# Kernel optimization log

Measured on AMD Instinct MI355X. Metric: run time of the kernel, lower is better.

The kernel has to match this reference:

```python
import jax, jax.numpy as jnp
import numpy as np

EMBED_DIM = 1024
NUM_HEADS = 16
HEAD_DIM = EMBED_DIM // NUM_HEADS


def setup_inputs() -> dict:
    key = jax.random.key(0)
    k1, k2, k3, k4, k5 = jax.random.split(key, 5)
    B, S, D = 1, 4096, EMBED_DIM
    scale = 0.02
    return {
        "input": jax.random.normal(k1, (B, S, D), dtype=jnp.float32),
        "Wqkv": jax.random.normal(k2, (D, 3 * D), dtype=jnp.float32) * scale,
        "bqkv": jax.random.normal(k3, (3 * D,), dtype=jnp.float32) * scale,
        "Wo": jax.random.normal(k4, (D, D), dtype=jnp.float32) * scale,
        "bo": jax.random.normal(k5, (D,), dtype=jnp.float32) * scale,
    }


def reference(input, Wqkv, bqkv, Wo, bo):
    B, S, D = input.shape
    H, Hd = NUM_HEADS, HEAD_DIM
    qkv = input @ Wqkv + bqkv                        # [B, S, 3D]
    qkv = qkv.reshape(B, S, 3, H, Hd)
    qkv = jnp.transpose(qkv, (2, 0, 3, 1, 4))        # [3, B, H, S, Hd]
    q, k, v = qkv[0], qkv[1], qkv[2]
    scores = jnp.einsum("bhsd,bhtd->bhst", q, k) / (Hd ** 0.5)  # [B,H,S,S]
    causal = jnp.tril(jnp.ones((S, S), dtype=bool))[None, None]
    scores = jnp.where(causal, scores, -jnp.inf)
    attn = jax.nn.softmax(scores, axis=-1)
    out = jnp.einsum("bhst,bhtd->bhsd", attn, v)     # [B,H,S,Hd]
    out = jnp.transpose(out, (0, 2, 1, 3)).reshape(B, S, D)
    return out @ Wo + bo
```

## Files before the change

### kernel.cpp

```cpp
#include <hip/hip_runtime.h>

typedef __bf16 bf16;
typedef __bf16 bf16x8 __attribute__((ext_vector_type(8)));
typedef float f32x4 __attribute__((ext_vector_type(4)));
typedef float f32x16 __attribute__((ext_vector_type(16)));
typedef unsigned u32x2 __attribute__((ext_vector_type(2)));

#define MFMA16(a, b, c) __builtin_amdgcn_mfma_f32_16x16x32_bf16((a), (b), (c), 0, 0, 0)
#define MFMA32(a, b, c) __builtin_amdgcn_mfma_f32_32x32x16_bf16((a), (b), (c), 0, 0, 0)

typedef const __attribute__((address_space(1))) uint32_t glb_u32;
typedef __attribute__((address_space(3))) uint32_t lds_u32;
#define GLOAD16(gp, lp) __builtin_amdgcn_global_load_lds((glb_u32*)(gp), (lds_u32*)(lp), 16, 0, 0)

__global__ __launch_bounds__(256) void k_prep(const float* __restrict__ X, bf16* __restrict__ Xb,
                                              const float* __restrict__ Wqkv, bf16* __restrict__ WqkvT,
                                              const float* __restrict__ Wo, bf16* __restrict__ WoT) {
    __shared__ float tile[64][65];
    int bid = blockIdx.x;
    int t = threadIdx.x;
    if (bid < 2048) {
        size_t i = ((size_t)bid * 256 + t) * 8;
        float4 a = *(const float4*)(X + i);
        float4 b = *(const float4*)(X + i + 4);
        bf16 e[8];
        e[0] = (bf16)a.x; e[1] = (bf16)a.y; e[2] = (bf16)a.z; e[3] = (bf16)a.w;
        e[4] = (bf16)b.x; e[5] = (bf16)b.y; e[6] = (bf16)b.z; e[7] = (bf16)b.w;
        uint4 u; __builtin_memcpy(&u, e, 16);
        *(uint4*)(Xb + i) = u;
        return;
    }
    const float* in; bf16* out; int R, C, bx, by;
    if (bid < 2816) {
        in = Wqkv; out = WqkvT; R = 1024; C = 3072;
        int b = bid - 2048; bx = b % 48; by = b / 48;
    } else {
        in = Wo; out = WoT; R = 1024; C = 1024;
        int b = bid - 2816; bx = b & 15; by = b >> 4;
    }
    for (int i = 0; i < 16; ++i) {
        int e = i * 256 + t; int r = e >> 6, c = e & 63;
        tile[r][c] = in[(size_t)(by * 64 + r) * C + bx * 64 + c];
    }
    __syncthreads();
    for (int i = 0; i < 16; ++i) {
        int e = i * 256 + t; int r = e >> 6, c = e & 63;
        out[(size_t)(bx * 64 + r) * R + by * 64 + c] = (bf16)tile[c][r];
    }
}

__device__ __forceinline__ void gemm128_core(const bf16* __restrict__ A, const bf16* __restrict__ Bt,
                                             int r0, int c0, int Kd, char* As, char* Bs,
                                             f32x4 (&acc)[4][4]) {
    int t = threadIdx.x, l = t & 63, w = t >> 6;
    int g = l >> 4, li = l & 15;
    int wr = w >> 1, wc = w & 1;
    for (int k0 = 0; k0 < Kd; k0 += 64) {
        __syncthreads();
        #pragma unroll
        for (int i = 0; i < 4; ++i) {
            int slot = i * 256 + t;
            int row = slot >> 3;
            int ch  = (slot & 7) ^ (row & 7);
            int base = (i * 256 + w * 64) * 16;
            GLOAD16(A  + (size_t)(r0 + row) * Kd + k0 + ch * 8, As + base);
            GLOAD16(Bt + (size_t)(c0 + row) * Kd + k0 + ch * 8, Bs + base);
        }
        __syncthreads();
        __builtin_amdgcn_s_setprio(1);
        #pragma unroll
        for (int kk = 0; kk < 2; ++kk) {
            bf16x8 af[4], bfr[4];
            #pragma unroll
            for (int m = 0; m < 4; ++m) {
                int row = wr * 64 + m * 16 + li;
                af[m] = *(const bf16x8*)(As + ((row * 128 + kk * 64 + g * 16) ^ ((row & 7) << 4)));
            }
            #pragma unroll
            for (int n = 0; n < 4; ++n) {
                int row = wc * 64 + n * 16 + li;
                bfr[n] = *(const bf16x8*)(Bs + ((row * 128 + kk * 64 + g * 16) ^ ((row & 7) << 4)));
            }
            #pragma unroll
            for (int m = 0; m < 4; ++m)
                #pragma unroll
                for (int n = 0; n < 4; ++n)
                    acc[m][n] = MFMA16(af[m], bfr[n], acc[m][n]);
        }
        __builtin_amdgcn_s_setprio(0);
    }
}

__global__ __launch_bounds__(256) void k_gemm_qkv(const bf16* __restrict__ Xb, const bf16* __restrict__ WqkvT,
                                                  const float* __restrict__ bqkv,
                                                  bf16* __restrict__ Q, bf16* __restrict__ Kfr,
                                                  bf16* __restrict__ Vfr) {
    __shared__ __align__(16) char As[16384];
    __shared__ __align__(16) char Bs[16384];
    int bid = blockIdx.x;
    int Lg = (bid & 7) * 96 + (bid >> 3);
    int bx = Lg % 24, by = Lg / 24;
    int r0 = by * 128, c0 = bx * 128;
    f32x4 acc[4][4] = {};
    gemm128_core(Xb, WqkvT, r0, c0, 1024, As, Bs, acc);
    int t = threadIdx.x, l = t & 63, w = t >> 6;
    int g = l >> 4, li = l & 15;
    int wr = w >> 1, wc = w & 1;
    int colbase = c0 + wc * 64;
    int sec = colbase >> 10;
    int head = (colbase & 1023) >> 6;
    if (sec == 0) {
        const float scale = 0.125f * 1.44269504f;
        #pragma unroll
        for (int m = 0; m < 4; ++m)
            #pragma unroll
            for (int n = 0; n < 4; ++n) {
                int hd = n * 16 + li;
                float bias = bqkv[colbase + hd];
                #pragma unroll
                for (int r = 0; r < 4; ++r) {
                    int row = r0 + wr * 64 + m * 16 + g * 4 + r;
                    Q[(size_t)(head * 4096 + row) * 64 + hd] = (bf16)((acc[m][n][r] + bias) * scale);
                }
            }
    } else if (sec == 1) {
        bf16* dstK = Kfr + (size_t)head * 262144;
        #pragma unroll
        for (int m = 0; m < 4; ++m) {
            int tbase = r0 + wr * 64 + m * 16 + g * 4;
            size_t tpart = (size_t)(tbase >> 5) * 2048 + (size_t)(tbase & 31) * 8;
            #pragma unroll
            for (int n = 0; n < 4; ++n) {
                int hd = n * 16 + li;
                float bias = bqkv[colbase + hd];
                size_t A0 = tpart + (size_t)(hd >> 4) * 512 + (size_t)((hd >> 3) & 1) * 256 + (hd & 7);
                #pragma unroll
                for (int r = 0; r < 4; ++r)
                    dstK[A0 + (size_t)r * 8] = (bf16)(acc[m][n][r] + bias);
            }
        }
    } else {
        bf16* dstV = Vfr + (size_t)head * 262144;
        #pragma unroll
        for (int m = 0; m < 4; ++m) {
            int tbase = r0 + wr * 64 + m * 16 + g * 4;
            size_t tpart = (size_t)(tbase >> 5) * 2048 + (size_t)((tbase >> 4) & 1) * 512
                         + (size_t)((tbase >> 3) & 1) * 256 + (tbase & 7);
            #pragma unroll
            for (int n = 0; n < 4; ++n) {
                int hd = n * 16 + li;
                float bias = bqkv[colbase + hd];
                size_t A0 = tpart + (size_t)(hd >> 5) * 1024 + (size_t)(hd & 31) * 8;
                bf16 e4[4];
                #pragma unroll
                for (int r = 0; r < 4; ++r) e4[r] = (bf16)(acc[m][n][r] + bias);
                unsigned long long pk; __builtin_memcpy(&pk, e4, 8);
                *(unsigned long long*)(dstV + A0) = pk;
            }
        }
    }
}

__global__ __launch_bounds__(256) void k_gemm_out(const bf16* __restrict__ Ob, const bf16* __restrict__ WoT,
                                                  const float* __restrict__ bo, float* __restrict__ out) {
    __shared__ __align__(16) char As[16384];
    __shared__ __align__(16) char Bs[8192];
    int bid = blockIdx.x;
    int Lg = (bid & 7) * 64 + (bid >> 3);
    int bx = Lg & 15, by = Lg >> 4;
    int r0 = by * 128, c0 = bx * 64;
    int t = threadIdx.x, l = t & 63, w = t >> 6;
    int g = l >> 4, li = l & 15;
    f32x4 acc[2][4] = {};
    for (int k0 = 0; k0 < 1024; k0 += 64) {
        __syncthreads();
        #pragma unroll
        for (int i = 0; i < 4; ++i) {
            int slot = i * 256 + t;
            int row = slot >> 3;
            int ch  = (slot & 7) ^ (row & 7);
            int base = (i * 256 + w * 64) * 16;
            GLOAD16(Ob + (size_t)(r0 + row) * 1024 + k0 + ch * 8, As + base);
        }
        #pragma unroll
        for (int i = 0; i < 2; ++i) {
            int slot = i * 256 + t;
            int row = slot >> 3;
            int ch  = (slot & 7) ^ (row & 7);
            int base = (i * 256 + w * 64) * 16;
            GLOAD16(WoT + (size_t)(c0 + row) * 1024 + k0 + ch * 8, Bs + base);
        }
        __syncthreads();
        __builtin_amdgcn_s_setprio(1);
        #pragma unroll
        for (int kk = 0; kk < 2; ++kk) {
            bf16x8 af[2], bfr[4];
            #pragma unroll
            for (int m = 0; m < 2; ++m) {
                int row = w * 32 + m * 16 + li;
                af[m] = *(const bf16x8*)(As + ((row * 128 + kk * 64 + g * 16) ^ ((row & 7) << 4)));
            }
            #pragma unroll
            for (int n = 0; n < 4; ++n) {
                int row = n * 16 + li;
                bfr[n] = *(const bf16x8*)(Bs + ((row * 128 + kk * 64 + g * 16) ^ ((row & 7) << 4)));
            }
            #pragma unroll
            for (int m = 0; m < 2; ++m)
                #pragma unroll
                for (int n = 0; n < 4; ++n)
                    acc[m][n] = MFMA16(af[m], bfr[n], acc[m][n]);
        }
        __builtin_amdgcn_s_setprio(0);
    }
    #pragma unroll
    for (int m = 0; m < 2; ++m)
        #pragma unroll
        for (int n = 0; n < 4; ++n) {
            int col = c0 + n * 16 + li;
            float bias = bo[col];
            #pragma unroll
            for (int r = 0; r < 4; ++r) {
                int row = r0 + w * 32 + m * 16 + g * 4 + r;
                out[(size_t)row * 1024 + col] = acc[m][n][r] + bias;
            }
        }
}

__device__ __forceinline__ unsigned pkbf(float a, float b) {
    bf16 h0 = (bf16)a, h1 = (bf16)b;
    unsigned short u0, u1;
    __builtin_memcpy(&u0, &h0, 2); __builtin_memcpy(&u1, &h1, 2);
    return (unsigned)u0 | ((unsigned)u1 << 16);
}

__global__ __launch_bounds__(128) void k_attn(const bf16* __restrict__ Q, const uint4* __restrict__ Kfr,
                                              const uint4* __restrict__ Vfr, bf16* __restrict__ O) {
    __shared__ float Op[32][64];
    __shared__ float Ls[32];
    int bid = blockIdx.x;
    int h = bid & 15;
    int u = bid >> 4;
    int jj = (u < 64) ? u : 191 - u;
    int w = threadIdx.x >> 6;
    int l = threadIdx.x & 63;
    int lc = l & 31, hi = l >> 5;
    int hi4 = hi * 4, hi8 = hi * 8;
    const bf16* Qh = Q + (size_t)h * 4096 * 64;
    const uint4* Kh = Kfr + (size_t)h * 32768;
    const uint4* Vh = Vfr + (size_t)h * 32768;
    int nt = jj + 1;
    int hA = (nt + 1) >> 1;
    int tb = w ? hA : 0;
    int te = w ? nt : hA;

    f32x16 oacc[2] = {};
    float lsum = 0.f;
    uint4 kA[4], vA[4], kB[4], vB[4];
    bf16x8 qf[4];
    #pragma unroll
    for (int kst = 0; kst < 4; ++kst)
        qf[kst] = *(const bf16x8*)(Qh + (size_t)(jj * 32 + lc) * 64 + kst * 16 + hi8);

    auto compute = [&](int tt, uint4 (&kf)[4], uint4 (&vf)[4]) {
        f32x16 sacc = {};
        __builtin_amdgcn_s_setprio(1);
        #pragma unroll
        for (int kst = 0; kst < 4; ++kst) {
            bf16x8 kk; __builtin_memcpy(&kk, &kf[kst], 16);
            sacc = MFMA32(kk, qf[kst], sacc);
        }
        __builtin_amdgcn_s_setprio(0);
        if (tt == jj) {
            #pragma unroll
            for (int r = 0; r < 16; ++r) {
                int tloc = (r & 3) + 8 * (r >> 2) + hi4;
                if (tloc > lc) sacc[r] = -1e30f;
            }
        }
        float pv[16];
        float rs0 = 0.f, rs1 = 0.f;
        #pragma unroll
        for (int r = 0; r < 8; ++r) {
            pv[r]     = exp2f(sacc[r]);     rs0 += pv[r];
            pv[r + 8] = exp2f(sacc[r + 8]); rs1 += pv[r + 8];
        }
        lsum += rs0 + rs1;
        #pragma unroll
        for (int ks = 0; ks < 2; ++ks) {
            int b = ks * 8;
            unsigned a0 = pkbf(pv[b + 0], pv[b + 1]), a1 = pkbf(pv[b + 2], pv[b + 3]);
            unsigned b0 = pkbf(pv[b + 4], pv[b + 5]), b1 = pkbf(pv[b + 6], pv[b + 7]);
            u32x2 r0 = __builtin_amdgcn_permlane32_swap(a0, b0, false, false);
            u32x2 r1 = __builtin_amdgcn_permlane32_swap(a1, b1, false, false);
            unsigned wsq[4] = { r0[0], r1[0], r0[1], r1[1] };
            bf16x8 pa; __builtin_memcpy(&pa, wsq, 16);
            __builtin_amdgcn_s_setprio(1);
            #pragma unroll
            for (int jt = 0; jt < 2; ++jt) {
                bf16x8 vv; __builtin_memcpy(&vv, &vf[jt * 2 + ks], 16);
                oacc[jt] = MFMA32(pa, vv, oacc[jt]);
            }
            __builtin_amdgcn_s_setprio(0);
        }
    };

    if (te > tb) {
        #pragma unroll
        for (int i = 0; i < 4; ++i) {
            kA[i] = Kh[(size_t)tb * 256 + i * 64 + l];
            vA[i] = Vh[(size_t)tb * 256 + i * 64 + l];
        }
        int i = tb;
        for (; i + 2 <= te; i += 2) {
            const uint4* Kn = Kh + (size_t)(i + 1) * 256;
            const uint4* Vn = Vh + (size_t)(i + 1) * 256;
            #pragma unroll
            for (int q = 0; q < 4; ++q) { kB[q] = Kn[q * 64 + l]; vB[q] = Vn[q * 64 + l]; }
            compute(i, kA, vA);
            if (i + 2 < te) {
                const uint4* K2 = Kh + (size_t)(i + 2) * 256;
                const uint4* V2 = Vh + (size_t)(i + 2) * 256;
                #pragma unroll
                for (int q = 0; q < 4; ++q) { kA[q] = K2[q * 64 + l]; vA[q] = V2[q * 64 + l]; }
            }
            compute(i + 1, kB, vB);
        }
        if ((te - tb) & 1) compute(te - 1, kA, vA);
    }
    lsum += __shfl_xor(lsum, 32);

    if (w == 1) {
        #pragma unroll
        for (int r = 0; r < 16; ++r) {
            int ql = (r & 3) + 8 * (r >> 2) + hi4;
            Op[ql][lc]      = oacc[0][r];
            Op[ql][32 + lc] = oacc[1][r];
        }
        if (hi == 0) Ls[lc] = lsum;
    }
    __syncthreads();
    if (w == 0) {
        float inv = 1.0f / (lsum + Ls[lc]);
        int q0 = jj * 32;
        #pragma unroll
        for (int r = 0; r < 16; ++r) {
            int ql = (r & 3) + 8 * (r >> 2) + hi4;
            float ib = __shfl(inv, ql);
            float o0 = (oacc[0][r] + Op[ql][lc])      * ib;
            float o1 = (oacc[1][r] + Op[ql][32 + lc]) * ib;
            int row = q0 + ql;
            O[(size_t)row * 1024 + h * 64 + lc]      = (bf16)o0;
            O[(size_t)row * 1024 + h * 64 + 32 + lc] = (bf16)o1;
        }
    }
}

extern "C" void kernel_launch(void* const* d_in, const int* in_sizes, int n_in,
                              void* d_out, int out_size, void* d_ws, size_t ws_size,
                              hipStream_t stream) {
    const float* X    = (const float*)d_in[0];
    const float* Wqkv = (const float*)d_in[1];
    const float* bqkv = (const float*)d_in[2];
    const float* Wo   = (const float*)d_in[3];
    const float* bo   = (const float*)d_in[4];
    float* out = (float*)d_out;

    char* ws = (char*)d_ws;
    const size_t MB = 1024 * 1024;
    bf16*  Xb    = (bf16*)(ws);
    bf16*  WqkvT = (bf16*)(ws + 8  * MB);
    bf16*  WoT   = (bf16*)(ws + 14 * MB);
    bf16*  Qb    = (bf16*)(ws + 16 * MB);
    uint4* Kfr   = (uint4*)(ws + 40 * MB);
    uint4* Vfr   = (uint4*)(ws + 48 * MB);
    bf16*  Ob    = Xb;

    k_prep<<<3072, 256, 0, stream>>>(X, Xb, Wqkv, WqkvT, Wo, WoT);
    k_gemm_qkv<<<768, 256, 0, stream>>>(Xb, WqkvT, bqkv, Qb, (bf16*)Kfr, (bf16*)Vfr);
    k_attn<<<2048, 128, 0, stream>>>(Qb, Kfr, Vfr, Ob);
    k_gemm_out<<<512, 256, 0, stream>>>(Ob, WoT, bo, out);
}
```

Baseline: 137.5 us.

## Pair complementary causal query tiles per attention block to balance work

Each attention block now processes two query tiles, p and 127-p, so every block does the same total number of KV tiles. Each wave handles half of one tile's KV range and half of the other's, and the partial results are exchanged through a doubled shared-memory buffer before both waves write output. This halves the grid size and is meant to remove the triangular load imbalance and tail effects of the causal mask. In exchange there are fewer blocks, which may reduce occupancy and latency hiding.

```diff
diff --git a/kernel.cpp b/kernel.cpp
--- a/kernel.cpp
+++ b/kernel.cpp
@@ -236,12 +236,11 @@
 
 __global__ __launch_bounds__(128) void k_attn(const bf16* __restrict__ Q, const uint4* __restrict__ Kfr,
                                               const uint4* __restrict__ Vfr, bf16* __restrict__ O) {
-    __shared__ float Op[32][64];
-    __shared__ float Ls[32];
+    __shared__ float Op[2][32][64];
+    __shared__ float Ls[2][32];
     int bid = blockIdx.x;
     int h = bid & 15;
-    int u = bid >> 4;
-    int jj = (u < 64) ? u : 191 - u;
+    int p = bid >> 4;
     int w = threadIdx.x >> 6;
     int l = threadIdx.x & 63;
     int lc = l & 31, hi = l >> 5;
@@ -249,20 +248,18 @@
     const bf16* Qh = Q + (size_t)h * 4096 * 64;
     const uint4* Kh = Kfr + (size_t)h * 32768;
     const uint4* Vh = Vfr + (size_t)h * 32768;
-    int nt = jj + 1;
-    int hA = (nt + 1) >> 1;
-    int tb = w ? hA : 0;
-    int te = w ? nt : hA;
-
-    f32x16 oacc[2] = {};
-    float lsum = 0.f;
+    int jA = p, jB = 127 - p;
+    int ntA = jA + 1, ntB = jB + 1;
+    int hA = ntA >> 1, hB = ntB >> 1;
+    int j1 = w ? jA : jB, b1 = w ? hA : hB, e1 = w ? ntA : ntB;
+    int j2 = w ? jB : jA, e2 = w ? hB : hA;
+
+    f32x16 oacc[2];
+    float lsum;
     uint4 kA[4], vA[4], kB[4], vB[4];
     bf16x8 qf[4];
-    #pragma unroll
-    for (int kst = 0; kst < 4; ++kst)
-        qf[kst] = *(const bf16x8*)(Qh + (size_t)(jj * 32 + lc) * 64 + kst * 16 + hi8);
-
-    auto compute = [&](int tt, uint4 (&kf)[4], uint4 (&vf)[4]) {
+
+    auto compute = [&](int jjq, int tt, uint4 (&kf)[4], uint4 (&vf)[4]) {
         f32x16 sacc = {};
         __builtin_amdgcn_s_setprio(1);
         #pragma unroll
@@ -271,7 +268,7 @@
             sacc = MFMA32(kk, qf[kst], sacc);
         }
         __builtin_amdgcn_s_setprio(0);
-        if (tt == jj) {
+        if (tt == jjq) {
             #pragma unroll
             for (int r = 0; r < 16; ++r) {
                 int tloc = (r & 3) + 8 * (r >> 2) + hi4;
@@ -290,9 +287,9 @@
         for (int ks = 0; ks < 2; ++ks) {
             int b = ks * 8;
             unsigned a0 = pkbf(pv[b + 0], pv[b + 1]), a1 = pkbf(pv[b + 2], pv[b + 3]);
-            unsigned b0 = pkbf(pv[b + 4], pv[b + 5]), b1 = pkbf(pv[b + 6], pv[b + 7]);
+            unsigned b0 = pkbf(pv[b + 4], pv[b + 5]), b1v = pkbf(pv[b + 6], pv[b + 7]);
             u32x2 r0 = __builtin_amdgcn_permlane32_swap(a0, b0, false, false);
-            u32x2 r1 = __builtin_amdgcn_permlane32_swap(a1, b1, false, false);
+            u32x2 r1 = __builtin_amdgcn_permlane32_swap(a1, b1v, false, false);
             unsigned wsq[4] = { r0[0], r1[0], r0[1], r1[1] };
             bf16x8 pa; __builtin_memcpy(&pa, wsq, 16);
             __builtin_amdgcn_s_setprio(1);
@@ -305,7 +302,8 @@
         }
     };
 
-    if (te > tb) {
+    auto runseg = [&](int jjq, int tb, int te) {
+        if (te <= tb) return;
         #pragma unroll
         for (int i = 0; i < 4; ++i) {
             kA[i] = Kh[(size_t)tb * 256 + i * 64 + l];
@@ -317,42 +315,57 @@
             const uint4* Vn = Vh + (size_t)(i + 1) * 256;
             #pragma unroll
             for (int q = 0; q < 4; ++q) { kB[q] = Kn[q * 64 + l]; vB[q] = Vn[q * 64 + l]; }
-            compute(i, kA, vA);
+            compute(jjq, i, kA, vA);
             if (i + 2 < te) {
                 const uint4* K2 = Kh + (size_t)(i + 2) * 256;
                 const uint4* V2 = Vh + (size_t)(i + 2) * 256;
                 #pragma unroll
                 for (int q = 0; q < 4; ++q) { kA[q] = K2[q * 64 + l]; vA[q] = V2[q * 64 + l]; }
             }
-            compute(i + 1, kB, vB);
-        }
-        if ((te - tb) & 1) compute(te - 1, kA, vA);
-    }
+            compute(jjq, i + 1, kB, vB);
+        }
+        if ((te - tb) & 1) compute(jjq, te - 1, kA, vA);
+    };
+
+    #pragma unroll
+    for (int kst = 0; kst < 4; ++kst)
+        qf[kst] = *(const bf16x8*)(Qh + (size_t)(j1 * 32 + lc) * 64 + kst * 16 + hi8);
+    lsum = 0.f;
+    #pragma unroll
+    for (int r = 0; r < 16; ++r) { oacc[0][r] = 0.f; oacc[1][r] = 0.f; }
+    runseg(j1, b1, e1);
     lsum += __shfl_xor(lsum, 32);
-
-    if (w == 1) {
-        #pragma unroll
-        for (int r = 0; r < 16; ++r) {
-            int ql = (r & 3) + 8 * (r >> 2) + hi4;
-            Op[ql][lc]      = oacc[0][r];
-            Op[ql][32 + lc] = oacc[1][r];
-        }
-        if (hi == 0) Ls[lc] = lsum;
-    }
+    #pragma unroll
+    for (int r = 0; r < 16; ++r) {
+        int ql = (r & 3) + 8 * (r >> 2) + hi4;
+        Op[w][ql][lc]      = oacc[0][r];
+        Op[w][ql][32 + lc] = oacc[1][r];
+    }
+    if (hi == 0) Ls[w][lc] = lsum;
+
+    #pragma unroll
+    for (int kst = 0; kst < 4; ++kst)
+        qf[kst] = *(const bf16x8*)(Qh + (size_t)(j2 * 32 + lc) * 64 + kst * 16 + hi8);
+    lsum = 0.f;
+    #pragma unroll
+    for (int r = 0; r < 16; ++r) { oacc[0][r] = 0.f; oacc[1][r] = 0.f; }
+    runseg(j2, 0, e2);
+    lsum += __shfl_xor(lsum, 32);
+
     __syncthreads();
-    if (w == 0) {
-        float inv = 1.0f / (lsum + Ls[lc]);
-        int q0 = jj * 32;
-        #pragma unroll
-        for (int r = 0; r < 16; ++r) {
-            int ql = (r & 3) + 8 * (r >> 2) + hi4;
-            float ib = __shfl(inv, ql);
-            float o0 = (oacc[0][r] + Op[ql][lc])      * ib;
-            float o1 = (oacc[1][r] + Op[ql][32 + lc]) * ib;
-            int row = q0 + ql;
-            O[(size_t)row * 1024 + h * 64 + lc]      = (bf16)o0;
-            O[(size_t)row * 1024 + h * 64 + 32 + lc] = (bf16)o1;
-        }
+
+    int o = w ^ 1;
+    float inv = 1.0f / (lsum + Ls[o][lc]);
+    int q0 = j2 * 32;
+    #pragma unroll
+    for (int r = 0; r < 16; ++r) {
+        int ql = (r & 3) + 8 * (r >> 2) + hi4;
+        float ib = __shfl(inv, ql);
+        float o0 = (oacc[0][r] + Op[o][ql][lc])      * ib;
+        float o1 = (oacc[1][r] + Op[o][ql][32 + lc]) * ib;
+        int row = q0 + ql;
+        O[(size_t)row * 1024 + h * 64 + lc]      = (bf16)o0;
+        O[(size_t)row * 1024 + h * 64 + 32 + lc] = (bf16)o1;
     }
 }
 
@@ -378,6 +391,6 @@
 
     k_prep<<<3072, 256, 0, stream>>>(X, Xb, Wqkv, WqkvT, Wo, WoT);
     k_gemm_qkv<<<768, 256, 0, stream>>>(Xb, WqkvT, bqkv, Qb, (bf16*)Kfr, (bf16*)Vfr);
-    k_attn<<<2048, 128, 0, stream>>>(Qb, Kfr, Vfr, Ob);
+    k_attn<<<1024, 128, 0, stream>>>(Qb, Kfr, Vfr, Ob);
     k_gemm_out<<<512, 256, 0, stream>>>(Ob, WoT, bo, out);
 }
```

After: 138.1 us. About the same (+0.4%).
